# Optimization experiments

Hardware: AMD Instinct MI355X
Metric: run time of the kernel (lower is better)

## Reference

```python
import jax, jax.numpy as jnp
import numpy as np
import math

# ShiftedL2Loss constants derived from init kwargs
SAMPLE_RATE = 48000
ALPHA = 100.0
MAX_DIST = 1.5
DIST_SAMPLES = int(SAMPLE_RATE * MAX_DIST / 340)  # 211
T_WIN = 2 ** int(math.floor(math.log(DIST_SAMPLES, 2)))  # t = 128
S_SHIFTS = T_WIN * 2 + 1                                  # S = 257
T_BIG = T_WIN + S_SHIFTS - 1                              # T = 384
DT = T_WIN                                                # dT = t


def _blackman_window(M):
    # torch.blackman_window(M, periodic=False)
    n = jnp.arange(M, dtype=jnp.float32)
    denom = jnp.float32(M - 1)
    return (0.42 - 0.5 * jnp.cos(2.0 * jnp.pi * n / denom)
            + 0.08 * jnp.cos(4.0 * jnp.pi * n / denom))


def setup_inputs() -> dict:
    key = jax.random.key(0)
    k1, k2 = jax.random.split(key)
    B, C, L = 4, 8, 15104  # L = 118 * 128 -> exact tiling
    data = jax.random.normal(k1, (B, C, L), dtype=jnp.float32)
    target = jax.random.normal(k2, (B, C, L), dtype=jnp.float32)
    return {"data": data, "target": target}


def reference(data, target):
    t, S = T_WIN, S_SHIFTS
    w = ALPHA * (1.0 - _blackman_window(S))  # (S,)

    # flatten to (BC, L)
    x = data.reshape(-1, data.shape[-1])
    r = target.reshape(-1, target.shape[-1])
    L = x.shape[-1]
    N = (L - t) // DT + 1
    Ltrim = (N - 1) * DT + t
    x = x[:, :Ltrim]
    r = r[:, :Ltrim]

    # magnitude normalization on the center region
    d = x[:, t:-t]
    rc = r[:, t:-t]
    d = d - jnp.mean(d, axis=1, keepdims=True)
    rc = rc - jnp.mean(rc, axis=1, keepdims=True)
    mag_x = jnp.sqrt(jnp.mean(d ** 2, axis=1, keepdims=True))
    mag_r = jnp.sqrt(jnp.mean(rc ** 2, axis=1, keepdims=True))
    mag_min = jnp.minimum(mag_x, mag_r)
    mag_norm = jnp.sqrt(mag_min * mag_r) + 0.001  # (BC, 1)
    x = x / mag_norm
    r = r / mag_norm

    # zero-pad reference by t on both sides
    r_pad = jnp.pad(r, ((0, 0), (t, t)))  # (BC, Ltrim + 2t)

    # non-overlapping predicted windows: (BC, N, t)
    xw = x.reshape(-1, N, t)

    # shifted reference windows: (BC, N, S, t)
    starts = (jnp.arange(N) * DT)[:, None, None]
    idx = starts + jnp.arange(S)[None, :, None] + jnp.arange(t)[None, None, :]
    yw = r_pad[:, idx]  # gather -> (BC, N, S, t)

    # per-shift MSE over the window: (BC, N, S)
    mse = jnp.mean((xw[:, :, None, :] - yw) ** 2, axis=-1)

    # shift-weighted penalty, min over shifts, mean over everything
    loss = (mse + 1.0) * (w[None, None, :] + 1.0) - 1.0
    loss = jnp.amin(loss, axis=-1)  # (BC, N)
    return jnp.mean(loss).reshape(1)
```

## Files before the change

kernel.cpp:

```cpp
#include <hip/hip_runtime.h>
#include <math.h>

#define ROWS 32
#define LROW 15104
#define TWIN 128
#define NWIN 118
#define TRIM 14848
#define NW   (ROWS * NWIN)
#define WPB  8
#define BPR  15
#define NBLK (ROWS * BPR)
#define XPAN (WPB * TWIN)
#define YPAN ((WPB + 3) * TWIN)

__global__ __launch_bounds__(512) void loss_fused(
        const float* __restrict__ data,
        const float* __restrict__ target,
        float* __restrict__ blocksums) {
    int b0 = blockIdx.x;
    int b  = (b0 & 7) * (NBLK / 8) + (b0 >> 3);
    int row = b / BPR;
    int n0  = (b % BPR) * WPB;
    int tid  = threadIdx.x;
    int wave = tid >> 6;
    int lane = tid & 63;

    __shared__ float xs[XPAN];
    __shared__ float ys[YPAN];
    __shared__ float4 wsum[8];
    __shared__ float s_scale;
    __shared__ float wl[8];

    const float* xrow = data   + row * LROW;
    const float* rrow = target + row * LROW;

    {
        const float4* x4 = (const float4*)(xrow + TWIN);
        const float4* r4 = (const float4*)(rrow + TWIN);
        float sd = 0.f, sd2 = 0.f, sr = 0.f, sr2 = 0.f;
        for (int i = tid; i < TRIM / 4; i += 512) {
            float4 a = x4[i], bv = r4[i];
            sd  += a.x + a.y + a.z + a.w;
            sd2 += a.x*a.x + a.y*a.y + a.z*a.z + a.w*a.w;
            sr  += bv.x + bv.y + bv.z + bv.w;
            sr2 += bv.x*bv.x + bv.y*bv.y + bv.z*bv.z + bv.w*bv.w;
        }
        #pragma unroll
        for (int off = 32; off > 0; off >>= 1) {
            sd  += __shfl_xor(sd,  off, 64);
            sd2 += __shfl_xor(sd2, off, 64);
            sr  += __shfl_xor(sr,  off, 64);
            sr2 += __shfl_xor(sr2, off, 64);
        }
        if (lane == 0) wsum[wave] = make_float4(sd, sd2, sr, sr2);
    }
    __syncthreads();
    if (tid == 0) {
        float sd = 0.f, sd2 = 0.f, sr = 0.f, sr2 = 0.f;
        #pragma unroll
        for (int i = 0; i < 8; ++i) {
            float4 p = wsum[i];
            sd += p.x; sd2 += p.y; sr += p.z; sr2 += p.w;
        }
        const float inv = 1.0f / (float)TRIM;
        float md = sd * inv, mr = sr * inv;
        float vx = fmaxf(sd2 * inv - md * md, 0.f);
        float vr = fmaxf(sr2 * inv - mr * mr, 0.f);
        float mag_x = sqrtf(vx), mag_r = sqrtf(vr);
        float mag_min = fminf(mag_x, mag_r);
        s_scale = 1.0f / (sqrtf(mag_min * mag_r) + 0.001f);
    }
    __syncthreads();
    float scale = s_scale;

    for (int j = tid; j < XPAN / 4; j += 512) {
        int g = n0 * TWIN + 4 * j;
        float4 v = make_float4(0.f, 0.f, 0.f, 0.f);
        if (g < LROW) v = *(const float4*)(xrow + g);
        *(float4*)&xs[4 * j] =
            make_float4(v.x * scale, v.y * scale, v.z * scale, v.w * scale);
    }
    for (int j = tid; j < YPAN / 4; j += 512) {
        int g = (n0 - 1) * TWIN + 4 * j;
        float4 v = make_float4(0.f, 0.f, 0.f, 0.f);
        if (g >= 0 && g < LROW) v = *(const float4*)(rrow + g);
        *(float4*)&ys[4 * j] =
            make_float4(v.x * scale, v.y * scale, v.z * scale, v.w * scale);
    }
    __syncthreads();

    int n = n0 + wave;
    float lmin = 0.f;
    if (n < NWIN) {
        const float* xw = xs + wave * TWIN;
        const float* yw = ys + wave * TWIN;

        float sx, part;
        {
            float xa = xw[lane], xb = xw[lane + 64];
            float ya = yw[256 + lane], yb = yw[320 + lane];
            float d1 = xa - ya, d2 = xb - yb;
            part = d1 * d1 + d2 * d2;
            sx   = xa * xa + xb * xb;
            #pragma unroll
            for (int off = 32; off > 0; off >>= 1) {
                part += __shfl_xor(part, off, 64);
                sx   += __shfl_xor(sx,   off, 64);
            }
        }

        const float4* xs4 = (const float4*)xw;
        const float4* ys4 = (const float4*)yw;

        float4 yv0 = ys4[lane];
        float yf0 = yv0.x, yf1 = yv0.y, yf2 = yv0.z;
        float c0 = 0.f, c1 = 0.f, c2 = 0.f, c3 = 0.f;
        float q = 0.f;

        #pragma unroll
        for (int kb = 0; kb < 32; ++kb) {
            float4 xv  = xs4[kb];
            float4 yv1 = ys4[lane + kb + 1];
            c0 += xv.x*yv0.x + xv.y*yv0.y + xv.z*yv0.z + xv.w*yv0.w;
            c1 += xv.x*yv0.y + xv.y*yv0.z + xv.z*yv0.w + xv.w*yv1.x;
            c2 += xv.x*yv0.z + xv.y*yv0.w + xv.z*yv1.x + xv.w*yv1.y;
            c3 += xv.x*yv0.w + xv.y*yv1.x + xv.z*yv1.y + xv.w*yv1.z;
            q  += yv0.x*yv0.x + yv0.y*yv0.y + yv0.z*yv0.z + yv0.w*yv0.w;
            yv0 = yv1;
        }
        float sy0 = q;
        float sy1 = sy0 - yf0*yf0 + yv0.x*yv0.x;
        float sy2 = sy1 - yf1*yf1 + yv0.y*yv0.y;
        float sy3 = sy2 - yf2*yf2 + yv0.z*yv0.z;

        const float inv = 1.0f / (float)TWIN;
        int   s0  = lane * 4;
        lmin = 1e30f;
        {
            float mse, ph, cp, bw, w;
            mse = (sx - 2.f*c0 + sy0) * inv;
            ph  = (float)(s0 + 0) * (float)(M_PI / 128.0);
            cp  = __cosf(ph); bw = 0.42f - 0.5f*cp + 0.08f*(2.f*cp*cp - 1.f);
            w   = 100.f * (1.f - bw);
            lmin = fminf(lmin, (mse + 1.f) * (w + 1.f) - 1.f);
            mse = (sx - 2.f*c1 + sy1) * inv;
            ph  = (float)(s0 + 1) * (float)(M_PI / 128.0);
            cp  = __cosf(ph); bw = 0.42f - 0.5f*cp + 0.08f*(2.f*cp*cp - 1.f);
            w   = 100.f * (1.f - bw);
            lmin = fminf(lmin, (mse + 1.f) * (w + 1.f) - 1.f);
            mse = (sx - 2.f*c2 + sy2) * inv;
            ph  = (float)(s0 + 2) * (float)(M_PI / 128.0);
            cp  = __cosf(ph); bw = 0.42f - 0.5f*cp + 0.08f*(2.f*cp*cp - 1.f);
            w   = 100.f * (1.f - bw);
            lmin = fminf(lmin, (mse + 1.f) * (w + 1.f) - 1.f);
            mse = (sx - 2.f*c3 + sy3) * inv;
            ph  = (float)(s0 + 3) * (float)(M_PI / 128.0);
            cp  = __cosf(ph); bw = 0.42f - 0.5f*cp + 0.08f*(2.f*cp*cp - 1.f);
            w   = 100.f * (1.f - bw);
            lmin = fminf(lmin, (mse + 1.f) * (w + 1.f) - 1.f);
        }
        {
            float mse256 = part * inv;
            lmin = fminf(lmin, (mse256 + 1.f) * 101.f - 1.f);
        }
        #pragma unroll
        for (int off = 32; off > 0; off >>= 1)
            lmin = fminf(lmin, __shfl_xor(lmin, off, 64));
    }

    if (lane == 0) wl[wave] = lmin;
    __syncthreads();
    if (tid == 0) {
        float s = 0.f;
        #pragma unroll
        for (int i = 0; i < 8; ++i) s += wl[i];
        blocksums[b] = s;
    }
}

__global__ __launch_bounds__(256) void finish_kernel(
        const float* __restrict__ blocksums,
        float* __restrict__ out) {
    int tid = threadIdx.x;
    float s = 0.f;
    for (int i = tid; i < NBLK; i += 256) s += blocksums[i];
    __shared__ float sh[256];
    sh[tid] = s;
    __syncthreads();
    for (int off = 128; off > 0; off >>= 1) {
        if (tid < off) sh[tid] += sh[tid + off];
        __syncthreads();
    }
    if (tid == 0) out[0] = sh[0] / (float)NW;
}

extern "C" void kernel_launch(void* const* d_in, const int* in_sizes, int n_in,
                              void* d_out, int out_size, void* d_ws, size_t ws_size,
                              hipStream_t stream) {
    const float* data   = (const float*)d_in[0];
    const float* target = (const float*)d_in[1];
    float* blocksums = (float*)d_ws;

    loss_fused<<<NBLK, 512, 0, stream>>>(data, target, blocksums);
    finish_kernel<<<1, 256, 0, stream>>>(blocksums, (float*)d_out);
}
```

Before: 18.39 us.

## Overlap row normalization with correlation via dedicated stats wave and deferred scaling

Dedicates wave 0 to computing the row mean/variance normalization while waves 1-7 compute unscaled cross-correlations concurrently. The scale is applied afterwards as scale² on the MSE, since the loss is quadratic in the inputs, which removes a barrier and the scaling pass over the panels. The x window now lives in registers and is broadcast with readlane instead of going through shared memory. Blocks now handle 7 windows each (17 per row), and a single wave does the full stats reduction, which may lengthen the critical path. A __syncthreads inside divergent branches relies on barrier-count matching across waves.

```diff
diff --git a/kernel.cpp b/kernel.cpp
--- a/kernel.cpp
+++ b/kernel.cpp
@@ -7,11 +7,14 @@
 #define NWIN 118
 #define TRIM 14848
 #define NW   (ROWS * NWIN)
-#define WPB  8
-#define BPR  15
+#define WPB  7
+#define BPR  17
 #define NBLK (ROWS * BPR)
-#define XPAN (WPB * TWIN)
-#define YPAN ((WPB + 3) * TWIN)
+#define YPAN ((WPB + 2) * TWIN)
+
+__device__ __forceinline__ float readlane_f(float v, int lane) {
+    return __int_as_float(__builtin_amdgcn_readlane(__float_as_int(v), lane));
+}
 
 __global__ __launch_bounds__(512) void loss_fused(
         const float* __restrict__ data,
@@ -25,20 +28,37 @@
     int wave = tid >> 6;
     int lane = tid & 63;
 
-    __shared__ float xs[XPAN];
     __shared__ float ys[YPAN];
-    __shared__ float4 wsum[8];
-    __shared__ float s_scale;
     __shared__ float wl[8];
+    __shared__ float s_scale2;
 
     const float* xrow = data   + row * LROW;
     const float* rrow = target + row * LROW;
 
-    {
+    int  n     = n0 + wave - 1;
+    bool valid = (wave >= 1) && (n < NWIN);
+
+    float xa = 0.f, xb = 0.f;
+    if (valid) {
+        float2 v = *(const float2*)(xrow + n * TWIN + 2 * lane);
+        xa = v.x; xb = v.y;
+    }
+
+    for (int j = tid; j < YPAN / 4; j += 512) {
+        int g = (n0 - 1) * TWIN + 4 * j;
+        float4 v = make_float4(0.f, 0.f, 0.f, 0.f);
+        if (g >= 0 && g < LROW) v = *(const float4*)(rrow + g);
+        *(float4*)&ys[4 * j] = v;
+    }
+    __syncthreads();
+
+    float lmin = 0.f;
+
+    if (wave == 0) {
         const float4* x4 = (const float4*)(xrow + TWIN);
         const float4* r4 = (const float4*)(rrow + TWIN);
         float sd = 0.f, sd2 = 0.f, sr = 0.f, sr2 = 0.f;
-        for (int i = tid; i < TRIM / 4; i += 512) {
+        for (int i = lane; i < TRIM / 4; i += 64) {
             float4 a = x4[i], bv = r4[i];
             sd  += a.x + a.y + a.z + a.w;
             sd2 += a.x*a.x + a.y*a.y + a.z*a.z + a.w*a.w;
@@ -52,55 +72,25 @@
             sr  += __shfl_xor(sr,  off, 64);
             sr2 += __shfl_xor(sr2, off, 64);
         }
-        if (lane == 0) wsum[wave] = make_float4(sd, sd2, sr, sr2);
-    }
-    __syncthreads();
-    if (tid == 0) {
-        float sd = 0.f, sd2 = 0.f, sr = 0.f, sr2 = 0.f;
-        #pragma unroll
-        for (int i = 0; i < 8; ++i) {
-            float4 p = wsum[i];
-            sd += p.x; sd2 += p.y; sr += p.z; sr2 += p.w;
+        if (lane == 0) {
+            const float inv = 1.0f / (float)TRIM;
+            float md = sd * inv, mr = sr * inv;
+            float vx = fmaxf(sd2 * inv - md * md, 0.f);
+            float vr = fmaxf(sr2 * inv - mr * mr, 0.f);
+            float mag_x = sqrtf(vx), mag_r = sqrtf(vr);
+            float mag_min = fminf(mag_x, mag_r);
+            float scale = 1.0f / (sqrtf(mag_min * mag_r) + 0.001f);
+            s_scale2 = scale * scale;
         }
-        const float inv = 1.0f / (float)TRIM;
-        float md = sd * inv, mr = sr * inv;
-        float vx = fmaxf(sd2 * inv - md * md, 0.f);
-        float vr = fmaxf(sr2 * inv - mr * mr, 0.f);
-        float mag_x = sqrtf(vx), mag_r = sqrtf(vr);
-        float mag_min = fminf(mag_x, mag_r);
-        s_scale = 1.0f / (sqrtf(mag_min * mag_r) + 0.001f);
-    }
-    __syncthreads();
-    float scale = s_scale;
-
-    for (int j = tid; j < XPAN / 4; j += 512) {
-        int g = n0 * TWIN + 4 * j;
-        float4 v = make_float4(0.f, 0.f, 0.f, 0.f);
-        if (g < LROW) v = *(const float4*)(xrow + g);
-        *(float4*)&xs[4 * j] =
-            make_float4(v.x * scale, v.y * scale, v.z * scale, v.w * scale);
-    }
-    for (int j = tid; j < YPAN / 4; j += 512) {
-        int g = (n0 - 1) * TWIN + 4 * j;
-        float4 v = make_float4(0.f, 0.f, 0.f, 0.f);
-        if (g >= 0 && g < LROW) v = *(const float4*)(rrow + g);
-        *(float4*)&ys[4 * j] =
-            make_float4(v.x * scale, v.y * scale, v.z * scale, v.w * scale);
-    }
-    __syncthreads();
-
-    int n = n0 + wave;
-    float lmin = 0.f;
-    if (n < NWIN) {
-        const float* xw = xs + wave * TWIN;
-        const float* yw = ys + wave * TWIN;
+    } else if (valid) {
+        const float*  yw  = ys + (wave - 1) * TWIN;
+        const float4* ys4 = (const float4*)yw;
 
         float sx, part;
         {
-            float xa = xw[lane], xb = xw[lane + 64];
-            float ya = yw[256 + lane], yb = yw[320 + lane];
-            float d1 = xa - ya, d2 = xb - yb;
-            part = d1 * d1 + d2 * d2;
+            float2 yv = *(const float2*)(yw + 256 + 2 * lane);
+            float d0 = xa - yv.x, d1 = xb - yv.y;
+            part = d0 * d0 + d1 * d1;
             sx   = xa * xa + xb * xb;
             #pragma unroll
             for (int off = 32; off > 0; off >>= 1) {
@@ -109,9 +99,6 @@
             }
         }
 
-        const float4* xs4 = (const float4*)xw;
-        const float4* ys4 = (const float4*)yw;
-
         float4 yv0 = ys4[lane];
         float yf0 = yv0.x, yf1 = yv0.y, yf2 = yv0.z;
         float c0 = 0.f, c1 = 0.f, c2 = 0.f, c3 = 0.f;
@@ -119,12 +106,15 @@
 
         #pragma unroll
         for (int kb = 0; kb < 32; ++kb) {
-            float4 xv  = xs4[kb];
+            float x0 = readlane_f(xa, 2 * kb);
+            float x1 = readlane_f(xb, 2 * kb);
+            float x2 = readlane_f(xa, 2 * kb + 1);
+            float x3 = readlane_f(xb, 2 * kb + 1);
             float4 yv1 = ys4[lane + kb + 1];
-            c0 += xv.x*yv0.x + xv.y*yv0.y + xv.z*yv0.z + xv.w*yv0.w;
-            c1 += xv.x*yv0.y + xv.y*yv0.z + xv.z*yv0.w + xv.w*yv1.x;
-            c2 += xv.x*yv0.z + xv.y*yv0.w + xv.z*yv1.x + xv.w*yv1.y;
-            c3 += xv.x*yv0.w + xv.y*yv1.x + xv.z*yv1.y + xv.w*yv1.z;
+            c0 += x0*yv0.x + x1*yv0.y + x2*yv0.z + x3*yv0.w;
+            c1 += x0*yv0.y + x1*yv0.z + x2*yv0.w + x3*yv1.x;
+            c2 += x0*yv0.z + x1*yv0.w + x2*yv1.x + x3*yv1.y;
+            c3 += x0*yv0.w + x1*yv1.x + x2*yv1.y + x3*yv1.z;
             q  += yv0.x*yv0.x + yv0.y*yv0.y + yv0.z*yv0.z + yv0.w*yv0.w;
             yv0 = yv1;
         }
@@ -133,47 +123,49 @@
         float sy2 = sy1 - yf1*yf1 + yv0.y*yv0.y;
         float sy3 = sy2 - yf2*yf2 + yv0.z*yv0.z;
 
+        __syncthreads();
+        float scale2 = s_scale2;
+
         const float inv = 1.0f / (float)TWIN;
         int   s0  = lane * 4;
         lmin = 1e30f;
         {
             float mse, ph, cp, bw, w;
-            mse = (sx - 2.f*c0 + sy0) * inv;
+            mse = scale2 * (sx - 2.f*c0 + sy0) * inv;
             ph  = (float)(s0 + 0) * (float)(M_PI / 128.0);
             cp  = __cosf(ph); bw = 0.42f - 0.5f*cp + 0.08f*(2.f*cp*cp - 1.f);
             w   = 100.f * (1.f - bw);
             lmin = fminf(lmin, (mse + 1.f) * (w + 1.f) - 1.f);
-            mse = (sx - 2.f*c1 + sy1) * inv;
+            mse = scale2 * (sx - 2.f*c1 + sy1) * inv;
             ph  = (float)(s0 + 1) * (float)(M_PI / 128.0);
             cp  = __cosf(ph); bw = 0.42f - 0.5f*cp + 0.08f*(2.f*cp*cp - 1.f);
             w   = 100.f * (1.f - bw);
             lmin = fminf(lmin, (mse + 1.f) * (w + 1.f) - 1.f);
-            mse = (sx - 2.f*c2 + sy2) * inv;
+            mse = scale2 * (sx - 2.f*c2 + sy2) * inv;
             ph  = (float)(s0 + 2) * (float)(M_PI / 128.0);
             cp  = __cosf(ph); bw = 0.42f - 0.5f*cp + 0.08f*(2.f*cp*cp - 1.f);
             w   = 100.f * (1.f - bw);
             lmin = fminf(lmin, (mse + 1.f) * (w + 1.f) - 1.f);
-            mse = (sx - 2.f*c3 + sy3) * inv;
+            mse = scale2 * (sx - 2.f*c3 + sy3) * inv;
             ph  = (float)(s0 + 3) * (float)(M_PI / 128.0);
             cp  = __cosf(ph); bw = 0.42f - 0.5f*cp + 0.08f*(2.f*cp*cp - 1.f);
             w   = 100.f * (1.f - bw);
             lmin = fminf(lmin, (mse + 1.f) * (w + 1.f) - 1.f);
         }
-        {
-            float mse256 = part * inv;
-            lmin = fminf(lmin, (mse256 + 1.f) * 101.f - 1.f);
-        }
+        lmin = fminf(lmin, (scale2 * part * inv + 1.f) * 101.f - 1.f);
         #pragma unroll
         for (int off = 32; off > 0; off >>= 1)
             lmin = fminf(lmin, __shfl_xor(lmin, off, 64));
     }
+
+    if (wave == 0 || !valid) __syncthreads();
 
     if (lane == 0) wl[wave] = lmin;
     __syncthreads();
     if (tid == 0) {
         float s = 0.f;
         #pragma unroll
-        for (int i = 0; i < 8; ++i) s += wl[i];
+        for (int i = 1; i < 8; ++i) s += wl[i];
         blocksums[b] = s;
     }
 }
```

After: 26.24 us. 42.7% more time.

## Apply normalization scale post-hoc and read x windows directly from global memory

Applied to the files above, without the earlier changes.

The kernel no longer scales the inputs by the normalization factor. Since MSE is quadratic, the per-shift sums are computed on raw data and multiplied by scale² at the end. This removes one block barrier and the tid-0 serial scale step, since every thread now reduces the wave partial sums itself. It also drops the x shared-memory panel and loads each wave's x window straight from global memory using a wave-uniform address, and shrinks the y panel to 10 windows. The risks are extra uniform global loads inside the inner loop in place of LDS reads, and small floating-point differences from the reordered scaling.

```diff
diff --git a/kernel.cpp b/kernel.cpp
--- a/kernel.cpp
+++ b/kernel.cpp
@@ -10,8 +10,7 @@
 #define WPB  8
 #define BPR  15
 #define NBLK (ROWS * BPR)
-#define XPAN (WPB * TWIN)
-#define YPAN ((WPB + 3) * TWIN)
+#define YPAN (10 * TWIN)
 
 __global__ __launch_bounds__(512) void loss_fused(
         const float* __restrict__ data,
@@ -25,19 +24,17 @@
     int wave = tid >> 6;
     int lane = tid & 63;
 
-    __shared__ float xs[XPAN];
-    __shared__ float ys[YPAN];
+    __shared__ float  ys[YPAN];
     __shared__ float4 wsum[8];
-    __shared__ float s_scale;
-    __shared__ float wl[8];
+    __shared__ float  wl[8];
 
     const float* xrow = data   + row * LROW;
     const float* rrow = target + row * LROW;
 
+    float sd = 0.f, sd2 = 0.f, sr = 0.f, sr2 = 0.f;
     {
         const float4* x4 = (const float4*)(xrow + TWIN);
         const float4* r4 = (const float4*)(rrow + TWIN);
-        float sd = 0.f, sd2 = 0.f, sr = 0.f, sr2 = 0.f;
         for (int i = tid; i < TRIM / 4; i += 512) {
             float4 a = x4[i], bv = r4[i];
             sd  += a.x + a.y + a.z + a.w;
@@ -54,119 +51,109 @@
         }
         if (lane == 0) wsum[wave] = make_float4(sd, sd2, sr, sr2);
     }
-    __syncthreads();
-    if (tid == 0) {
-        float sd = 0.f, sd2 = 0.f, sr = 0.f, sr2 = 0.f;
-        #pragma unroll
-        for (int i = 0; i < 8; ++i) {
-            float4 p = wsum[i];
-            sd += p.x; sd2 += p.y; sr += p.z; sr2 += p.w;
-        }
-        const float inv = 1.0f / (float)TRIM;
-        float md = sd * inv, mr = sr * inv;
-        float vx = fmaxf(sd2 * inv - md * md, 0.f);
-        float vr = fmaxf(sr2 * inv - mr * mr, 0.f);
-        float mag_x = sqrtf(vx), mag_r = sqrtf(vr);
-        float mag_min = fminf(mag_x, mag_r);
-        s_scale = 1.0f / (sqrtf(mag_min * mag_r) + 0.001f);
-    }
-    __syncthreads();
-    float scale = s_scale;
 
-    for (int j = tid; j < XPAN / 4; j += 512) {
-        int g = n0 * TWIN + 4 * j;
-        float4 v = make_float4(0.f, 0.f, 0.f, 0.f);
-        if (g < LROW) v = *(const float4*)(xrow + g);
-        *(float4*)&xs[4 * j] =
-            make_float4(v.x * scale, v.y * scale, v.z * scale, v.w * scale);
-    }
     for (int j = tid; j < YPAN / 4; j += 512) {
         int g = (n0 - 1) * TWIN + 4 * j;
         float4 v = make_float4(0.f, 0.f, 0.f, 0.f);
         if (g >= 0 && g < LROW) v = *(const float4*)(rrow + g);
-        *(float4*)&ys[4 * j] =
-            make_float4(v.x * scale, v.y * scale, v.z * scale, v.w * scale);
+        *(float4*)&ys[4 * j] = v;
     }
     __syncthreads();
 
-    int n = n0 + wave;
-    float lmin = 0.f;
-    if (n < NWIN) {
-        const float* xw = xs + wave * TWIN;
-        const float* yw = ys + wave * TWIN;
+    float scale2;
+    {
+        float td = 0.f, td2 = 0.f, tr = 0.f, tr2 = 0.f;
+        #pragma unroll
+        for (int i = 0; i < 8; ++i) {
+            float4 p = wsum[i];
+            td += p.x; td2 += p.y; tr += p.z; tr2 += p.w;
+        }
+        const float inv = 1.0f / (float)TRIM;
+        float md = td * inv, mr = tr * inv;
+        float vx = fmaxf(td2 * inv - md * md, 0.f);
+        float vr = fmaxf(tr2 * inv - mr * mr, 0.f);
+        float mag_x = sqrtf(vx), mag_r = sqrtf(vr);
+        float mag_min = fminf(mag_x, mag_r);
+        float scale = 1.0f / (sqrtf(mag_min * mag_r) + 0.001f);
+        scale2 = scale * scale;
+    }
 
-        float sx, part;
-        {
-            float xa = xw[lane], xb = xw[lane + 64];
-            float ya = yw[256 + lane], yb = yw[320 + lane];
-            float d1 = xa - ya, d2 = xb - yb;
-            part = d1 * d1 + d2 * d2;
-            sx   = xa * xa + xb * xb;
-            #pragma unroll
-            for (int off = 32; off > 0; off >>= 1) {
-                part += __shfl_xor(part, off, 64);
-                sx   += __shfl_xor(sx,   off, 64);
-            }
+    int  n     = n0 + wave;
+    bool valid = (n < NWIN);
+    int  nu    = __builtin_amdgcn_readfirstlane(valid ? n : NWIN - 1);
+    const float* xw = xrow + nu * TWIN;
+    const float* yw = ys + wave * TWIN;
+
+    float sx, part;
+    {
+        float xa = xw[lane], xb = xw[lane + 64];
+        float ya = yw[256 + lane], yb = yw[320 + lane];
+        float d0 = xa - ya, d1 = xb - yb;
+        part = d0 * d0 + d1 * d1;
+        sx   = xa * xa + xb * xb;
+        #pragma unroll
+        for (int off = 32; off > 0; off >>= 1) {
+            part += __shfl_xor(part, off, 64);
+            sx   += __shfl_xor(sx,   off, 64);
         }
+    }
 
-        const float4* xs4 = (const float4*)xw;
-        const float4* ys4 = (const float4*)yw;
+    const float4* ys4 = (const float4*)yw;
 
-        float4 yv0 = ys4[lane];
-        float yf0 = yv0.x, yf1 = yv0.y, yf2 = yv0.z;
-        float c0 = 0.f, c1 = 0.f, c2 = 0.f, c3 = 0.f;
-        float q = 0.f;
+    float4 yv0 = ys4[lane];
+    float yf0 = yv0.x, yf1 = yv0.y, yf2 = yv0.z;
+    float c0 = 0.f, c1 = 0.f, c2 = 0.f, c3 = 0.f;
+    float q = 0.f;
 
-        #pragma unroll
-        for (int kb = 0; kb < 32; ++kb) {
-            float4 xv  = xs4[kb];
-            float4 yv1 = ys4[lane + kb + 1];
-            c0 += xv.x*yv0.x + xv.y*yv0.y + xv.z*yv0.z + xv.w*yv0.w;
-            c1 += xv.x*yv0.y + xv.y*yv0.z + xv.z*yv0.w + xv.w*yv1.x;
-            c2 += xv.x*yv0.z + xv.y*yv0.w + xv.z*yv1.x + xv.w*yv1.y;
-            c3 += xv.x*yv0.w + xv.y*yv1.x + xv.z*yv1.y + xv.w*yv1.z;
-            q  += yv0.x*yv0.x + yv0.y*yv0.y + yv0.z*yv0.z + yv0.w*yv0.w;
-            yv0 = yv1;
-        }
-        float sy0 = q;
-        float sy1 = sy0 - yf0*yf0 + yv0.x*yv0.x;
-        float sy2 = sy1 - yf1*yf1 + yv0.y*yv0.y;
-        float sy3 = sy2 - yf2*yf2 + yv0.z*yv0.z;
+    #pragma unroll
+    for (int kb = 0; kb < 32; ++kb) {
+        float4 xv  = *(const float4*)(xw + 4 * kb);
+        float4 yv1 = ys4[lane + kb + 1];
+        c0 += xv.x*yv0.x + xv.y*yv0.y + xv.z*yv0.z + xv.w*yv0.w;
+        c1 += xv.x*yv0.y + xv.y*yv0.z + xv.z*yv0.w + xv.w*yv1.x;
+        c2 += xv.x*yv0.z + xv.y*yv0.w + xv.z*yv1.x + xv.w*yv1.y;
+        c3 += xv.x*yv0.w + xv.y*yv1.x + xv.z*yv1.y + xv.w*yv1.z;
+        q  += yv0.x*yv0.x + yv0.y*yv0.y + yv0.z*yv0.z + yv0.w*yv0.w;
+        yv0 = yv1;
+    }
+    float sy0 = q;
+    float sy1 = sy0 - yf0*yf0 + yv0.x*yv0.x;
+    float sy2 = sy1 - yf1*yf1 + yv0.y*yv0.y;
+    float sy3 = sy2 - yf2*yf2 + yv0.z*yv0.z;
 
-        const float inv = 1.0f / (float)TWIN;
-        int   s0  = lane * 4;
-        lmin = 1e30f;
-        {
-            float mse, ph, cp, bw, w;
-            mse = (sx - 2.f*c0 + sy0) * inv;
-            ph  = (float)(s0 + 0) * (float)(M_PI / 128.0);
-            cp  = __cosf(ph); bw = 0.42f - 0.5f*cp + 0.08f*(2.f*cp*cp - 1.f);
-            w   = 100.f * (1.f - bw);
-            lmin = fminf(lmin, (mse + 1.f) * (w + 1.f) - 1.f);
-            mse = (sx - 2.f*c1 + sy1) * inv;
-            ph  = (float)(s0 + 1) * (float)(M_PI / 128.0);
-            cp  = __cosf(ph); bw = 0.42f - 0.5f*cp + 0.08f*(2.f*cp*cp - 1.f);
-            w   = 100.f * (1.f - bw);
-            lmin = fminf(lmin, (mse + 1.f) * (w + 1.f) - 1.f);
-            mse = (sx - 2.f*c2 + sy2) * inv;
-            ph  = (float)(s0 + 2) * (float)(M_PI / 128.0);
-            cp  = __cosf(ph); bw = 0.42f - 0.5f*cp + 0.08f*(2.f*cp*cp - 1.f);
-            w   = 100.f * (1.f - bw);
-            lmin = fminf(lmin, (mse + 1.f) * (w + 1.f) - 1.f);
-            mse = (sx - 2.f*c3 + sy3) * inv;
-            ph  = (float)(s0 + 3) * (float)(M_PI / 128.0);
-            cp  = __cosf(ph); bw = 0.42f - 0.5f*cp + 0.08f*(2.f*cp*cp - 1.f);
-            w   = 100.f * (1.f - bw);
-            lmin = fminf(lmin, (mse + 1.f) * (w + 1.f) - 1.f);
-        }
-        {
-            float mse256 = part * inv;
-            lmin = fminf(lmin, (mse256 + 1.f) * 101.f - 1.f);
-        }
-        #pragma unroll
-        for (int off = 32; off > 0; off >>= 1)
-            lmin = fminf(lmin, __shfl_xor(lmin, off, 64));
+    const float inv = 1.0f / (float)TWIN;
+    int   s0  = lane * 4;
+    float lmin = 1e30f;
+    {
+        float mse, ph, cp, bw, w;
+        mse = scale2 * (sx - 2.f*c0 + sy0) * inv;
+        ph  = (float)(s0 + 0) * (float)(M_PI / 128.0);
+        cp  = __cosf(ph); bw = 0.42f - 0.5f*cp + 0.08f*(2.f*cp*cp - 1.f);
+        w   = 100.f * (1.f - bw);
+        lmin = fminf(lmin, (mse + 1.f) * (w + 1.f) - 1.f);
+        mse = scale2 * (sx - 2.f*c1 + sy1) * inv;
+        ph  = (float)(s0 + 1) * (float)(M_PI / 128.0);
+        cp  = __cosf(ph); bw = 0.42f - 0.5f*cp + 0.08f*(2.f*cp*cp - 1.f);
+        w   = 100.f * (1.f - bw);
+        lmin = fminf(lmin, (mse + 1.f) * (w + 1.f) - 1.f);
+        mse = scale2 * (sx - 2.f*c2 + sy2) * inv;
+        ph  = (float)(s0 + 2) * (float)(M_PI / 128.0);
+        cp  = __cosf(ph); bw = 0.42f - 0.5f*cp + 0.08f*(2.f*cp*cp - 1.f);
+        w   = 100.f * (1.f - bw);
+        lmin = fminf(lmin, (mse + 1.f) * (w + 1.f) - 1.f);
+        mse = scale2 * (sx - 2.f*c3 + sy3) * inv;
+        ph  = (float)(s0 + 3) * (float)(M_PI / 128.0);
+        cp  = __cosf(ph); bw = 0.42f - 0.5f*cp + 0.08f*(2.f*cp*cp - 1.f);
+        w   = 100.f * (1.f - bw);
+        lmin = fminf(lmin, (mse + 1.f) * (w + 1.f) - 1.f);
     }
+    lmin = fminf(lmin, (scale2 * part * inv + 1.f) * 101.f - 1.f);
+
+    #pragma unroll
+    for (int off = 32; off > 0; off >>= 1)
+        lmin = fminf(lmin, __shfl_xor(lmin, off, 64));
+
+    if (!valid) lmin = 0.f;
 
     if (lane == 0) wl[wave] = lmin;
     __syncthreads();
```

Result: faster. 17.23 us (-6.3%).
